# Optimization experiments

Measured on AMD Instinct MI355X. Metric: run time of the kernel, lower is better.

Reference implementation:

```python
import jax, jax.numpy as jnp
import numpy as np

H = 1024      # hidden_size
V = 50257     # output_size (vocab)
L = 64        # max_length


def setup_inputs() -> dict:
    key = jax.random.key(0)
    ks = jax.random.split(key, 14)
    s = 1.0 / np.sqrt(H)
    return {
        "input": jax.random.randint(ks[0], (1,), 0, V, dtype=jnp.int64),
        "hidden": jax.random.normal(ks[1], (1, 1, H), dtype=jnp.float32),
        "encoder_outputs": jax.random.normal(ks[2], (L, H), dtype=jnp.float32),
        "emb": jax.random.normal(ks[3], (V, H), dtype=jnp.float32),
        "attn_W": jax.random.normal(ks[4], (L, 2 * H), dtype=jnp.float32) * s,
        "attn_b": jax.random.normal(ks[5], (L,), dtype=jnp.float32) * s,
        "comb_W": jax.random.normal(ks[6], (H, 2 * H), dtype=jnp.float32) * s,
        "comb_b": jax.random.normal(ks[7], (H,), dtype=jnp.float32) * s,
        "w_ih": jax.random.normal(ks[8], (3 * H, H), dtype=jnp.float32) * s,
        "w_hh": jax.random.normal(ks[9], (3 * H, H), dtype=jnp.float32) * s,
        "b_ih": jax.random.normal(ks[10], (3 * H,), dtype=jnp.float32) * s,
        "b_hh": jax.random.normal(ks[11], (3 * H,), dtype=jnp.float32) * s,
        "out_W": jax.random.normal(ks[12], (V, H), dtype=jnp.float32) * s,
        "out_b": jax.random.normal(ks[13], (V,), dtype=jnp.float32) * s,
    }


def reference(input, hidden, encoder_outputs, emb, attn_W, attn_b,
              comb_W, comb_b, w_ih, w_hh, b_ih, b_hh, out_W, out_b):
    # embedded: [1, H]  (dropout is identity, p effectively 0 at inference)
    embedded = emb[input[0]][None, :]
    h0 = hidden[0]  # [1, H]

    # additive-style attention over encoder_outputs [L, H]
    attn_logits = jnp.concatenate([embedded, h0], axis=1) @ attn_W.T + attn_b  # [1, L]
    attn_weights = jax.nn.softmax(attn_logits, axis=1)                          # [1, L]
    attn_applied = attn_weights @ encoder_outputs                               # [1, H]

    x = jnp.concatenate([embedded, attn_applied], axis=1) @ comb_W.T + comb_b  # [1, H]
    x = jax.nn.relu(x)

    # single-step GRU cell (PyTorch gate ordering: r, z, n)
    gi = x @ w_ih.T + b_ih    # [1, 3H]
    gh = h0 @ w_hh.T + b_hh   # [1, 3H]
    i_r, i_z, i_n = jnp.split(gi, 3, axis=1)
    h_r, h_z, h_n = jnp.split(gh, 3, axis=1)
    r = jax.nn.sigmoid(i_r + h_r)
    z = jax.nn.sigmoid(i_z + h_z)
    n = jnp.tanh(i_n + r * h_n)
    h_new = (1.0 - z) * n + z * h0  # [1, H]

    out = jax.nn.log_softmax(h_new @ out_W.T + out_b, axis=1)  # [1, V]
    return out, h_new[None, :, :], attn_weights
```

## Files before the change

kernel.cpp:

```cpp
#include <hip/hip_runtime.h>
#include <math.h>

constexpr int H = 1024;
constexpr int V = 50257;
constexpr int L = 64;

constexpr int OFF_ALOG = 0;
constexpr int OFF_GH   = 64;
constexpr int OFF_X    = 64 + 3 * H;
constexpr int OFF_LOG  = OFF_X + H;
constexpr int NBLKD    = (V + 15) / 16;
constexpr int OFF_PAIR = OFF_LOG + V;

__device__ __forceinline__ float wave_reduce(float acc) {
    for (int off = 32; off > 0; off >>= 1) acc += __shfl_down(acc, off);
    return acc;
}

__device__ __forceinline__ float dot4(float4 a, float4 b) {
    return a.x * b.x + a.y * b.y + a.z * b.z + a.w * b.w;
}

__global__ __launch_bounds__(256) void kA(const int* __restrict__ idx_p,
                                          const float* __restrict__ hid,
                                          const float* __restrict__ emb,
                                          const float* __restrict__ attn_W,
                                          const float* __restrict__ attn_b,
                                          const float* __restrict__ w_hh,
                                          const float* __restrict__ b_hh,
                                          float* __restrict__ ws) {
    const int tid = threadIdx.x;
    const int lane = tid & 63, wid = tid >> 6;
    if (blockIdx.x < 64) {
        const int l = blockIdx.x;
        const int idx = idx_p[0];
        const float4* w4 = reinterpret_cast<const float4*>(attn_W + (size_t)l * (2 * H));
        const float4* e4 = reinterpret_cast<const float4*>(emb + (size_t)idx * H);
        const float4* h4 = reinterpret_cast<const float4*>(hid);
        float acc = dot4(w4[tid], e4[tid]) + dot4(w4[tid + 256], h4[tid]);
        acc = wave_reduce(acc);
        __shared__ float sred[4];
        if (lane == 0) sred[wid] = acc;
        __syncthreads();
        if (tid == 0)
            ws[OFF_ALOG + l] = sred[0] + sred[1] + sred[2] + sred[3] + attn_b[l];
    } else {
        __shared__ float4 sv[256];
        sv[tid] = reinterpret_cast<const float4*>(hid)[tid];
        __syncthreads();
        const int row = (blockIdx.x - 64) * 4 + wid;
        const float4* w4 = reinterpret_cast<const float4*>(w_hh + (size_t)row * H);
        float acc = 0.f;
#pragma unroll
        for (int it = 0; it < 4; ++it)
            acc += dot4(w4[lane + it * 64], sv[lane + it * 64]);
        acc = wave_reduce(acc);
        if (lane == 0) ws[OFF_GH + row] = acc + b_hh[row];
    }
}

__global__ __launch_bounds__(256) void kB(const int* __restrict__ idx_p,
                                          const float* __restrict__ emb,
                                          const float* __restrict__ enc,
                                          const float* __restrict__ comb_W,
                                          const float* __restrict__ comb_b,
                                          float* __restrict__ ws,
                                          float* __restrict__ out) {
    __shared__ float slog[L];
    __shared__ float wls[L];
    __shared__ float4 sx[512];
    const int tid = threadIdx.x;
    if (tid < L) slog[tid] = ws[OFF_ALOG + tid];
    __syncthreads();
    if (tid < L) {
        float m = -INFINITY;
        for (int i = 0; i < L; ++i) m = fmaxf(m, slog[i]);
        float s = 0.f;
        for (int i = 0; i < L; ++i) s += expf(slog[i] - m);
        wls[tid] = expf(slog[tid] - m) / s;
        if (blockIdx.x == 0) out[V + H + tid] = wls[tid];
    }
    __syncthreads();
    const int idx = idx_p[0];
    sx[tid] = reinterpret_cast<const float4*>(emb + (size_t)idx * H)[tid];
    {
        const float4* e4 = reinterpret_cast<const float4*>(enc);
        float4 acc4 = {0.f, 0.f, 0.f, 0.f};
#pragma unroll 8
        for (int l = 0; l < L; ++l) {
            const float w = wls[l];
            const float4 v = e4[l * 256 + tid];
            acc4.x += w * v.x; acc4.y += w * v.y;
            acc4.z += w * v.z; acc4.w += w * v.w;
        }
        sx[256 + tid] = acc4;
    }
    __syncthreads();
    const int lane = tid & 63, wid = tid >> 6;
    const int row = blockIdx.x * 4 + wid;
    const float4* w4 = reinterpret_cast<const float4*>(comb_W + (size_t)row * (2 * H));
    float acc = 0.f;
#pragma unroll
    for (int it = 0; it < 8; ++it)
        acc += dot4(w4[lane + it * 64], sx[lane + it * 64]);
    acc = wave_reduce(acc);
    if (lane == 0) ws[OFF_X + row] = fmaxf(acc + comb_b[row], 0.f);
}

__global__ __launch_bounds__(768) void kC(const float* __restrict__ w_ih,
                                          const float* __restrict__ b_ih,
                                          const float* __restrict__ hid,
                                          float* __restrict__ ws,
                                          float* __restrict__ out) {
    __shared__ float4 sx4[256];
    __shared__ float gi_s[12];
    const int tid = threadIdx.x;
    if (tid < 256) sx4[tid] = reinterpret_cast<const float4*>(ws + OFF_X)[tid];
    __syncthreads();
    const int lane = tid & 63, wid = tid >> 6;
    const int g = wid >> 2, i = wid & 3;
    const int row = g * H + blockIdx.x * 4 + i;
    const float4* w4 = reinterpret_cast<const float4*>(w_ih + (size_t)row * H);
    float acc = 0.f;
#pragma unroll
    for (int it = 0; it < 4; ++it)
        acc += dot4(w4[lane + it * 64], sx4[lane + it * 64]);
    acc = wave_reduce(acc);
    if (lane == 0) gi_s[wid] = acc + b_ih[row];
    __syncthreads();
    if (tid < 4) {
        const int t = blockIdx.x * 4 + tid;
        const float ir = gi_s[tid], iz = gi_s[4 + tid], in_ = gi_s[8 + tid];
        const float hr = ws[OFF_GH + t];
        const float hz = ws[OFF_GH + H + t];
        const float hn = ws[OFF_GH + 2 * H + t];
        const float r = 1.f / (1.f + expf(-(ir + hr)));
        const float z = 1.f / (1.f + expf(-(iz + hz)));
        const float n = tanhf(in_ + r * hn);
        out[V + t] = (1.f - z) * n + z * hid[t];
    }
}

__global__ __launch_bounds__(1024) void kD(const float* __restrict__ out_W,
                                           const float* __restrict__ out_b,
                                           const float* __restrict__ hnew,
                                           float* __restrict__ ws) {
    __shared__ float4 sh[256];
    __shared__ float srow[16];
    const int tid = threadIdx.x;
    if (tid < 256) sh[tid] = reinterpret_cast<const float4*>(hnew)[tid];
    __syncthreads();
    const int lane = tid & 63, wid = tid >> 6;
    const int row = blockIdx.x * 16 + wid;
    float logit = -INFINITY;
    if (row < V) {
        const float4* w4 = reinterpret_cast<const float4*>(out_W + (size_t)row * H);
        float acc = 0.f;
#pragma unroll
        for (int it = 0; it < 4; ++it)
            acc += dot4(w4[lane + it * 64], sh[lane + it * 64]);
        acc = wave_reduce(acc);
        if (lane == 0) {
            logit = acc + out_b[row];
            ws[OFF_LOG + row] = logit;
        }
    }
    if (lane == 0) srow[wid] = logit;
    __syncthreads();
    if (tid == 0) {
        float m = -INFINITY;
        for (int i = 0; i < 16; ++i) m = fmaxf(m, srow[i]);
        float s = 0.f;
        for (int i = 0; i < 16; ++i)
            if (srow[i] > -INFINITY) s += expf(srow[i] - m);
        ws[OFF_PAIR + 2 * blockIdx.x] = m;
        ws[OFF_PAIR + 2 * blockIdx.x + 1] = s;
    }
}

__global__ __launch_bounds__(256) void kE(const float* __restrict__ ws,
                                          float* __restrict__ out) {
    const int tid = threadIdx.x;
    float m = -INFINITY, s = 0.f;
    for (int i = tid; i < NBLKD; i += 256) {
        const float mi = ws[OFF_PAIR + 2 * i];
        const float si = ws[OFF_PAIR + 2 * i + 1];
        const float M = fmaxf(m, mi);
        s = s * expf(m - M) + si * expf(mi - M);
        m = M;
    }
    for (int off = 32; off > 0; off >>= 1) {
        const float mo = __shfl_down(m, off);
        const float so = __shfl_down(s, off);
        const float M = fmaxf(m, mo);
        s = s * expf(m - M) + so * expf(mo - M);
        m = M;
    }
    __shared__ float sm[4], ss[4];
    __shared__ float fin[2];
    const int lane = tid & 63, wid = tid >> 6;
    if (lane == 0) { sm[wid] = m; ss[wid] = s; }
    __syncthreads();
    if (tid == 0) {
        float M = sm[0], S = ss[0];
        for (int i = 1; i < 4; ++i) {
            const float Mn = fmaxf(M, sm[i]);
            S = S * expf(M - Mn) + ss[i] * expf(sm[i] - Mn);
            M = Mn;
        }
        fin[0] = M;
        fin[1] = logf(S);
    }
    __syncthreads();
    const int i = blockIdx.x * 256 + tid;
    if (i < V) out[i] = ws[OFF_LOG + i] - fin[0] - fin[1];
}

extern "C" void kernel_launch(void* const* d_in, const int* in_sizes, int n_in,
                              void* d_out, int out_size, void* d_ws, size_t ws_size,
                              hipStream_t stream) {
    const int*   idx    = (const int*)d_in[0];
    const float* hid    = (const float*)d_in[1];
    const float* enc    = (const float*)d_in[2];
    const float* emb    = (const float*)d_in[3];
    const float* attn_W = (const float*)d_in[4];
    const float* attn_b = (const float*)d_in[5];
    const float* comb_W = (const float*)d_in[6];
    const float* comb_b = (const float*)d_in[7];
    const float* w_ih   = (const float*)d_in[8];
    const float* w_hh   = (const float*)d_in[9];
    const float* b_ih   = (const float*)d_in[10];
    const float* b_hh   = (const float*)d_in[11];
    const float* out_W  = (const float*)d_in[12];
    const float* out_b  = (const float*)d_in[13];
    float* out = (float*)d_out;
    float* ws  = (float*)d_ws;

    kA<<<64 + 768, 256, 0, stream>>>(idx, hid, emb, attn_W, attn_b, w_hh, b_hh, ws);
    kB<<<256, 256, 0, stream>>>(idx, emb, enc, comb_W, comb_b, ws, out);
    kC<<<256, 768, 0, stream>>>(w_ih, b_ih, hid, ws, out);
    kD<<<NBLKD, 1024, 0, stream>>>(out_W, out_b, out + V, ws);
    kE<<<(V + 255) / 256, 256, 0, stream>>>(ws, out);
}
```

Measured before the change: 62.65 us.

## Restructure decoder into four kernels with redundant attention and fused GRU gates

Cuts the pipeline from five launches to four. Each front-kernel block now recomputes the 64 attention logits itself, and the w_hh gate projection moves into the GRU kernel so all six gate dot products for four hidden units are done together. The output projection now has each wave compute four rows with 256-thread blocks instead of one row per wave with 1024 threads, and the index is read as int64. In exchange, the 128 front blocks each redo the attention work, and the 3·H w_hh rows now sit on the serial chain after the combine step instead of running in the first kernel.

```diff
diff --git a/kernel.cpp b/kernel.cpp
--- a/kernel.cpp
+++ b/kernel.cpp
@@ -5,172 +5,204 @@
 constexpr int V = 50257;
 constexpr int L = 64;
 
-constexpr int OFF_ALOG = 0;
-constexpr int OFF_GH   = 64;
-constexpr int OFF_X    = 64 + 3 * H;
-constexpr int OFF_LOG  = OFF_X + H;
-constexpr int NBLKD    = (V + 15) / 16;
-constexpr int OFF_PAIR = OFF_LOG + V;
-
-__device__ __forceinline__ float wave_reduce(float acc) {
-    for (int off = 32; off > 0; off >>= 1) acc += __shfl_down(acc, off);
-    return acc;
+constexpr int NBLK3 = (V + 15) / 16;
+
+constexpr int OFF_X    = 0;
+constexpr int OFF_LOG  = 1024;
+constexpr int OFF_PAIR = 1024 + V;
+
+__device__ __forceinline__ float wsum(float v) {
+#pragma unroll
+    for (int off = 32; off > 0; off >>= 1) v += __shfl_xor(v, off);
+    return v;
+}
+__device__ __forceinline__ float wmax(float v) {
+#pragma unroll
+    for (int off = 32; off > 0; off >>= 1) v = fmaxf(v, __shfl_xor(v, off));
+    return v;
 }
 
 __device__ __forceinline__ float dot4(float4 a, float4 b) {
     return a.x * b.x + a.y * b.y + a.z * b.z + a.w * b.w;
 }
 
-__global__ __launch_bounds__(256) void kA(const int* __restrict__ idx_p,
-                                          const float* __restrict__ hid,
-                                          const float* __restrict__ emb,
-                                          const float* __restrict__ attn_W,
-                                          const float* __restrict__ attn_b,
-                                          const float* __restrict__ w_hh,
-                                          const float* __restrict__ b_hh,
-                                          float* __restrict__ ws) {
-    const int tid = threadIdx.x;
-    const int lane = tid & 63, wid = tid >> 6;
-    if (blockIdx.x < 64) {
-        const int l = blockIdx.x;
-        const int idx = idx_p[0];
-        const float4* w4 = reinterpret_cast<const float4*>(attn_W + (size_t)l * (2 * H));
-        const float4* e4 = reinterpret_cast<const float4*>(emb + (size_t)idx * H);
-        const float4* h4 = reinterpret_cast<const float4*>(hid);
-        float acc = dot4(w4[tid], e4[tid]) + dot4(w4[tid + 256], h4[tid]);
-        acc = wave_reduce(acc);
-        __shared__ float sred[4];
-        if (lane == 0) sred[wid] = acc;
-        __syncthreads();
-        if (tid == 0)
-            ws[OFF_ALOG + l] = sred[0] + sred[1] + sred[2] + sred[3] + attn_b[l];
-    } else {
-        __shared__ float4 sv[256];
-        sv[tid] = reinterpret_cast<const float4*>(hid)[tid];
-        __syncthreads();
-        const int row = (blockIdx.x - 64) * 4 + wid;
-        const float4* w4 = reinterpret_cast<const float4*>(w_hh + (size_t)row * H);
-        float acc = 0.f;
-#pragma unroll
-        for (int it = 0; it < 4; ++it)
-            acc += dot4(w4[lane + it * 64], sv[lane + it * 64]);
-        acc = wave_reduce(acc);
-        if (lane == 0) ws[OFF_GH + row] = acc + b_hh[row];
-    }
-}
-
-__global__ __launch_bounds__(256) void kB(const int* __restrict__ idx_p,
-                                          const float* __restrict__ emb,
-                                          const float* __restrict__ enc,
-                                          const float* __restrict__ comb_W,
-                                          const float* __restrict__ comb_b,
-                                          float* __restrict__ ws,
-                                          float* __restrict__ out) {
+__device__ __forceinline__ float dotN(const float* __restrict__ w,
+                                      const float* __restrict__ v,
+                                      int lane, int n4) {
+    const float4* w4 = reinterpret_cast<const float4*>(w);
+    const float4* v4 = reinterpret_cast<const float4*>(v);
+    float acc = 0.f;
+    for (int it = 0; it < n4; ++it)
+        acc += dot4(w4[lane + it * 64], v4[lane + it * 64]);
+    return acc;
+}
+
+__device__ __forceinline__ void dot1024x4(const float* __restrict__ w0,
+                                          const float* __restrict__ w1,
+                                          const float* __restrict__ w2,
+                                          const float* __restrict__ w3,
+                                          const float* __restrict__ v,
+                                          int lane, float* o) {
+    const float4* a4 = reinterpret_cast<const float4*>(w0);
+    const float4* b4 = reinterpret_cast<const float4*>(w1);
+    const float4* c4 = reinterpret_cast<const float4*>(w2);
+    const float4* d4 = reinterpret_cast<const float4*>(w3);
+    const float4* v4 = reinterpret_cast<const float4*>(v);
+    float s0 = 0.f, s1 = 0.f, s2 = 0.f, s3 = 0.f;
+#pragma unroll
+    for (int it = 0; it < 4; ++it) {
+        const float4 u = v4[lane + it * 64];
+        s0 += dot4(a4[lane + it * 64], u);
+        s1 += dot4(b4[lane + it * 64], u);
+        s2 += dot4(c4[lane + it * 64], u);
+        s3 += dot4(d4[lane + it * 64], u);
+    }
+    o[0] = s0; o[1] = s1; o[2] = s2; o[3] = s3;
+}
+
+__device__ __forceinline__ void msmerge(float& m, float& s, float m2, float s2) {
+    const float M = fmaxf(m, m2);
+    s = s * expf(m - M) + s2 * expf(m2 - M);
+    m = M;
+}
+
+__global__ __launch_bounds__(512) void k1_front(
+        const long long* __restrict__ idx_p,
+        const float* __restrict__ hid,
+        const float* __restrict__ enc,
+        const float* __restrict__ emb,
+        const float* __restrict__ attn_W,
+        const float* __restrict__ attn_b,
+        const float* __restrict__ comb_W,
+        const float* __restrict__ comb_b,
+        float* __restrict__ ws,
+        float* __restrict__ out) {
+    __shared__ __align__(16) float ecat[2 * H];
+    __shared__ __align__(16) float part[H];
     __shared__ float slog[L];
     __shared__ float wls[L];
-    __shared__ float4 sx[512];
-    const int tid = threadIdx.x;
-    if (tid < L) slog[tid] = ws[OFF_ALOG + tid];
-    __syncthreads();
-    if (tid < L) {
-        float m = -INFINITY;
-        for (int i = 0; i < L; ++i) m = fmaxf(m, slog[i]);
-        float s = 0.f;
-        for (int i = 0; i < L; ++i) s += expf(slog[i] - m);
-        wls[tid] = expf(slog[tid] - m) / s;
-        if (blockIdx.x == 0) out[V + H + tid] = wls[tid];
-    }
-    __syncthreads();
-    const int idx = idx_p[0];
-    sx[tid] = reinterpret_cast<const float4*>(emb + (size_t)idx * H)[tid];
+    const int tid = threadIdx.x, lane = tid & 63, wid = tid >> 6;
+    const int b = blockIdx.x;
+    const int idx = (int)idx_p[0];
+
+    for (int i = tid; i < H; i += 512) {
+        ecat[i]     = emb[(size_t)idx * H + i];
+        ecat[H + i] = hid[i];
+    }
+    __syncthreads();
+    for (int r = wid; r < L; r += 8) {
+        float acc = wsum(dotN(attn_W + (size_t)r * (2 * H), ecat, lane, 8));
+        if (lane == 0) slog[r] = acc + attn_b[r];
+    }
+    __syncthreads();
+    if (wid == 0) {
+        const float lg = slog[lane];
+        const float m = wmax(lg);
+        const float e = expf(lg - m);
+        const float s = wsum(e);
+        wls[lane] = e / s;
+        if (b == 0) out[V + H + lane] = e / s;
+    }
+    __syncthreads();
     {
         const float4* e4 = reinterpret_cast<const float4*>(enc);
-        float4 acc4 = {0.f, 0.f, 0.f, 0.f};
+        const int chunk = tid & 255, half = tid >> 8;
+        float4 a4 = {0.f, 0.f, 0.f, 0.f};
 #pragma unroll 8
-        for (int l = 0; l < L; ++l) {
-            const float w = wls[l];
-            const float4 v = e4[l * 256 + tid];
-            acc4.x += w * v.x; acc4.y += w * v.y;
-            acc4.z += w * v.z; acc4.w += w * v.w;
+        for (int l = half * 32; l < half * 32 + 32; ++l) {
+            const float wl = wls[l];
+            const float4 v = e4[l * 256 + chunk];
+            a4.x += wl * v.x; a4.y += wl * v.y; a4.z += wl * v.z; a4.w += wl * v.w;
         }
-        sx[256 + tid] = acc4;
-    }
-    __syncthreads();
-    const int lane = tid & 63, wid = tid >> 6;
-    const int row = blockIdx.x * 4 + wid;
-    const float4* w4 = reinterpret_cast<const float4*>(comb_W + (size_t)row * (2 * H));
-    float acc = 0.f;
-#pragma unroll
-    for (int it = 0; it < 8; ++it)
-        acc += dot4(w4[lane + it * 64], sx[lane + it * 64]);
-    acc = wave_reduce(acc);
-    if (lane == 0) ws[OFF_X + row] = fmaxf(acc + comb_b[row], 0.f);
-}
-
-__global__ __launch_bounds__(768) void kC(const float* __restrict__ w_ih,
-                                          const float* __restrict__ b_ih,
-                                          const float* __restrict__ hid,
-                                          float* __restrict__ ws,
-                                          float* __restrict__ out) {
-    __shared__ float4 sx4[256];
-    __shared__ float gi_s[12];
-    const int tid = threadIdx.x;
-    if (tid < 256) sx4[tid] = reinterpret_cast<const float4*>(ws + OFF_X)[tid];
-    __syncthreads();
-    const int lane = tid & 63, wid = tid >> 6;
-    const int g = wid >> 2, i = wid & 3;
-    const int row = g * H + blockIdx.x * 4 + i;
-    const float4* w4 = reinterpret_cast<const float4*>(w_ih + (size_t)row * H);
-    float acc = 0.f;
-#pragma unroll
-    for (int it = 0; it < 4; ++it)
-        acc += dot4(w4[lane + it * 64], sx4[lane + it * 64]);
-    acc = wave_reduce(acc);
-    if (lane == 0) gi_s[wid] = acc + b_ih[row];
+        if (half == 1) reinterpret_cast<float4*>(part)[chunk] = a4;
+        __syncthreads();
+        if (half == 0) {
+            const float4 p = reinterpret_cast<const float4*>(part)[chunk];
+            a4.x += p.x; a4.y += p.y; a4.z += p.z; a4.w += p.w;
+            reinterpret_cast<float4*>(ecat + H)[chunk] = a4;
+        }
+    }
+    __syncthreads();
+    {
+        const int r = b * 8 + wid;
+        float acc = wsum(dotN(comb_W + (size_t)r * (2 * H), ecat, lane, 8));
+        if (lane == 0) ws[OFF_X + r] = fmaxf(acc + comb_b[r], 0.f);
+    }
+}
+
+__global__ __launch_bounds__(512) void k2_gru(
+        const float* __restrict__ w_ih,
+        const float* __restrict__ w_hh,
+        const float* __restrict__ b_ih,
+        const float* __restrict__ b_hh,
+        const float* __restrict__ hid,
+        const float* __restrict__ ws,
+        float* __restrict__ out) {
+    __shared__ __align__(16) float sx[H];
+    __shared__ __align__(16) float sh[H];
+    __shared__ float gr[24];
+    const int tid = threadIdx.x, lane = tid & 63, wid = tid >> 6;
+    const int t0 = blockIdx.x * 4;
+    for (int i = tid; i < H; i += 512) {
+        sx[i] = ws[OFF_X + i];
+        sh[i] = hid[i];
+    }
+    __syncthreads();
+#pragma unroll
+    for (int q = 0; q < 3; ++q) {
+        const int k = wid + q * 8;
+        const int kk = (k < 12) ? k : k - 12;
+        const int g = kk >> 2, j = kk & 3;
+        const int row = g * H + t0 + j;
+        float acc;
+        if (k < 12) acc = wsum(dotN(w_ih + (size_t)row * H, sx, lane, 4)) + b_ih[row];
+        else        acc = wsum(dotN(w_hh + (size_t)row * H, sh, lane, 4)) + b_hh[row];
+        if (lane == 0) gr[k] = acc;
+    }
     __syncthreads();
     if (tid < 4) {
-        const int t = blockIdx.x * 4 + tid;
-        const float ir = gi_s[tid], iz = gi_s[4 + tid], in_ = gi_s[8 + tid];
-        const float hr = ws[OFF_GH + t];
-        const float hz = ws[OFF_GH + H + t];
-        const float hn = ws[OFF_GH + 2 * H + t];
+        const int j = tid;
+        const float ir = gr[j],      iz = gr[4 + j],  in_ = gr[8 + j];
+        const float hr = gr[12 + j], hz = gr[16 + j], hn  = gr[20 + j];
         const float r = 1.f / (1.f + expf(-(ir + hr)));
         const float z = 1.f / (1.f + expf(-(iz + hz)));
         const float n = tanhf(in_ + r * hn);
-        out[V + t] = (1.f - z) * n + z * hid[t];
-    }
-}
-
-__global__ __launch_bounds__(1024) void kD(const float* __restrict__ out_W,
-                                           const float* __restrict__ out_b,
-                                           const float* __restrict__ hnew,
-                                           float* __restrict__ ws) {
-    __shared__ float4 sh[256];
+        out[V + t0 + j] = (1.f - z) * n + z * sh[t0 + j];
+    }
+}
+
+__global__ __launch_bounds__(256, 4) void k3_outproj(
+        const float* __restrict__ out_W,
+        const float* __restrict__ out_b,
+        const float* __restrict__ hnew,
+        float* __restrict__ ws) {
+    __shared__ __align__(16) float shn[H];
     __shared__ float srow[16];
-    const int tid = threadIdx.x;
-    if (tid < 256) sh[tid] = reinterpret_cast<const float4*>(hnew)[tid];
-    __syncthreads();
-    const int lane = tid & 63, wid = tid >> 6;
-    const int row = blockIdx.x * 16 + wid;
-    float logit = -INFINITY;
-    if (row < V) {
-        const float4* w4 = reinterpret_cast<const float4*>(out_W + (size_t)row * H);
-        float acc = 0.f;
-#pragma unroll
-        for (int it = 0; it < 4; ++it)
-            acc += dot4(w4[lane + it * 64], sh[lane + it * 64]);
-        acc = wave_reduce(acc);
+    const int tid = threadIdx.x, lane = tid & 63, wid = tid >> 6;
+    for (int i = tid; i < H; i += 256) shn[i] = hnew[i];
+    __syncthreads();
+    const int row0 = blockIdx.x * 16 + wid * 4;
+    const int r0 = min(row0,     V - 1), r1 = min(row0 + 1, V - 1);
+    const int r2 = min(row0 + 2, V - 1), r3 = min(row0 + 3, V - 1);
+    float o[4];
+    dot1024x4(out_W + (size_t)r0 * H, out_W + (size_t)r1 * H,
+              out_W + (size_t)r2 * H, out_W + (size_t)r3 * H, shn, lane, o);
+#pragma unroll
+    for (int j = 0; j < 4; ++j) {
+        o[j] = wsum(o[j]);
         if (lane == 0) {
-            logit = acc + out_b[row];
-            ws[OFF_LOG + row] = logit;
+            const int r = row0 + j;
+            srow[wid * 4 + j] = (r < V) ? (o[j] + out_b[r]) : -INFINITY;
+            if (r < V) ws[OFF_LOG + r] = o[j] + out_b[r];
         }
     }
-    if (lane == 0) srow[wid] = logit;
     __syncthreads();
     if (tid == 0) {
         float m = -INFINITY;
+#pragma unroll
         for (int i = 0; i < 16; ++i) m = fmaxf(m, srow[i]);
         float s = 0.f;
+#pragma unroll
         for (int i = 0; i < 16; ++i)
             if (srow[i] > -INFINITY) s += expf(srow[i] - m);
         ws[OFF_PAIR + 2 * blockIdx.x] = m;
@@ -178,36 +210,28 @@
     }
 }
 
-__global__ __launch_bounds__(256) void kE(const float* __restrict__ ws,
-                                          float* __restrict__ out) {
-    const int tid = threadIdx.x;
+__global__ __launch_bounds__(256) void k4_write(const float* __restrict__ ws,
+                                                float* __restrict__ out) {
+    const int tid = threadIdx.x, lane = tid & 63, wid = tid >> 6;
     float m = -INFINITY, s = 0.f;
-    for (int i = tid; i < NBLKD; i += 256) {
+    for (int i = tid; i < NBLK3; i += 256) {
         const float mi = ws[OFF_PAIR + 2 * i];
         const float si = ws[OFF_PAIR + 2 * i + 1];
-        const float M = fmaxf(m, mi);
-        s = s * expf(m - M) + si * expf(mi - M);
-        m = M;
-    }
+        if (si > 0.f) msmerge(m, s, mi, si);
+    }
+#pragma unroll
     for (int off = 32; off > 0; off >>= 1) {
-        const float mo = __shfl_down(m, off);
-        const float so = __shfl_down(s, off);
-        const float M = fmaxf(m, mo);
-        s = s * expf(m - M) + so * expf(mo - M);
-        m = M;
-    }
-    __shared__ float sm[4], ss[4];
-    __shared__ float fin[2];
-    const int lane = tid & 63, wid = tid >> 6;
+        const float mo = __shfl_xor(m, off);
+        const float so = __shfl_xor(s, off);
+        if (so > 0.f) msmerge(m, s, mo, so);
+    }
+    __shared__ float sm[4], ss[4], fin[2];
     if (lane == 0) { sm[wid] = m; ss[wid] = s; }
     __syncthreads();
     if (tid == 0) {
         float M = sm[0], S = ss[0];
-        for (int i = 1; i < 4; ++i) {
-            const float Mn = fmaxf(M, sm[i]);
-            S = S * expf(M - Mn) + ss[i] * expf(sm[i] - Mn);
-            M = Mn;
-        }
+        for (int i = 1; i < 4; ++i)
+            if (ss[i] > 0.f) msmerge(M, S, sm[i], ss[i]);
         fin[0] = M;
         fin[1] = logf(S);
     }
@@ -219,7 +243,7 @@
 extern "C" void kernel_launch(void* const* d_in, const int* in_sizes, int n_in,
                               void* d_out, int out_size, void* d_ws, size_t ws_size,
                               hipStream_t stream) {
-    const int*   idx    = (const int*)d_in[0];
+    const long long* idx  = (const long long*)d_in[0];
     const float* hid    = (const float*)d_in[1];
     const float* enc    = (const float*)d_in[2];
     const float* emb    = (const float*)d_in[3];
@@ -236,9 +260,9 @@
     float* out = (float*)d_out;
     float* ws  = (float*)d_ws;
 
-    kA<<<64 + 768, 256, 0, stream>>>(idx, hid, emb, attn_W, attn_b, w_hh, b_hh, ws);
-    kB<<<256, 256, 0, stream>>>(idx, emb, enc, comb_W, comb_b, ws, out);
-    kC<<<256, 768, 0, stream>>>(w_ih, b_ih, hid, ws, out);
-    kD<<<NBLKD, 1024, 0, stream>>>(out_W, out_b, out + V, ws);
-    kE<<<(V + 255) / 256, 256, 0, stream>>>(ws, out);
-}
+    k1_front<<<128, 512, 0, stream>>>(idx, hid, enc, emb, attn_W, attn_b,
+                                      comb_W, comb_b, ws, out);
+    k2_gru<<<256, 512, 0, stream>>>(w_ih, w_hh, b_ih, b_hh, hid, ws, out);
+    k3_outproj<<<NBLK3, 256, 0, stream>>>(out_W, out_b, out + V, ws);
+    k4_write<<<(V + 255) / 256, 256, 0, stream>>>(ws, out);
+}
```

Result: slower. 68.83 us (+9.9%).
